# Optimization experiments

Measured on AMD Instinct MI355X. Metric: run time of the kernel, lower is better.

## Reference

```python
import jax, jax.numpy as jnp
import numpy as np

B, N, D_IN, D_OUT, R = 8, 1024, 256, 256, 4


def setup_inputs() -> dict:
    key = jax.random.key(0)
    ks = jax.random.split(key, 8)
    scale_in = 1.0 / np.sqrt(D_IN)
    scale_out = 1.0 / np.sqrt(2 * D_OUT)
    scale_g = 1.0 / np.sqrt(D_OUT)
    return {
        "node_features": jax.random.normal(ks[0], (B, N, D_IN), dtype=jnp.float32),
        "adj_matrix": jax.random.randint(ks[1], (B, R, N, N), 0, 2, dtype=jnp.int32),
        "rel_w": jax.random.uniform(ks[2], (R, D_OUT, D_IN), jnp.float32, -scale_in, scale_in),
        "rel_b": jax.random.uniform(ks[3], (R, D_OUT), jnp.float32, -scale_in, scale_in),
        "attn_w": jax.random.uniform(ks[4], (2 * D_OUT,), jnp.float32, -scale_out, scale_out),
        "attn_b": jax.random.uniform(ks[5], (), jnp.float32, -scale_out, scale_out),
        "gate_w": jax.random.uniform(ks[6], (D_OUT,), jnp.float32, -scale_g, scale_g),
        "gate_b": jax.random.uniform(ks[7], (), jnp.float32, -scale_g, scale_g),
    }


def reference(node_features, adj_matrix, rel_w, rel_b, attn_w, attn_b, gate_w, gate_b):
    # Per-relation projections: [B, R, N, D]
    feats = jnp.einsum('bni,rdi->brnd', node_features, rel_w) + rel_b[None, :, None, :]
    # attn_proj(cat([h_i, h_j])) == h_i @ w_i + h_j @ w_j + b  (linear over concat)
    d = feats.shape[-1]
    si = jnp.einsum('brnd,d->brn', feats, attn_w[:d])   # contribution of row node i
    sj = jnp.einsum('brnd,d->brn', feats, attn_w[d:])   # contribution of col node j
    score = si[:, :, :, None] + sj[:, :, None, :] + attn_b  # [B, R, N, N]
    score = jnp.where(adj_matrix == 0, jnp.float32(-1e9), score)
    attn = jax.nn.softmax(score, axis=-1)
    # Aggregate over relations: sum_r attn_r @ feats_r -> [B, N, D]
    agg = jnp.einsum('brnm,brmd->bnd', attn, feats)
    gate = jax.nn.sigmoid(jnp.einsum('bnd,d->bn', agg, gate_w) + gate_b)
    return gate[:, :, None] * agg
```

## Files before the change

kernel.cpp:

```cpp
#include <hip/hip_runtime.h>
#include <hip/hip_bf16.h>

#define B_ 8
#define N_ 1024
#define DIN 256
#define DOUT 256
#define R_ 4

typedef __attribute__((ext_vector_type(8))) short bf16x8;
typedef __attribute__((ext_vector_type(4))) float f32x4;
typedef __attribute__((ext_vector_type(4))) int i32x4;

__device__ __forceinline__ unsigned short f2bf(float f) {
    union { float f; unsigned int u; } v; v.f = f;
    unsigned int u = v.u;
    u += 0x7fffu + ((u >> 16) & 1u);
    return (unsigned short)(u >> 16);
}
__device__ __forceinline__ float bf2f(unsigned short h) {
    union { float f; unsigned int u; } v; v.u = ((unsigned int)h) << 16;
    return v.f;
}

__device__ __forceinline__ void gl_lds16(const void* g, void* l) {
    __builtin_amdgcn_global_load_lds(
        (const __attribute__((address_space(1))) unsigned int*)g,
        (__attribute__((address_space(3))) unsigned int*)l, 16, 0, 0);
}

__device__ __forceinline__ i32x4 gload4(const void* p) {
    i32x4 r;
    asm volatile("global_load_dwordx4 %0, %1, off" : "=v"(r) : "v"(p) : "memory");
    return r;
}

__global__ __launch_bounds__(256) void k0_swz(const float* __restrict__ rw,
                                              unsigned short* __restrict__ swzW) {
    int t = blockIdx.x * 256 + threadIdx.x;
    int lane = t & 63, nb = (t >> 6) & 15, ks = (t >> 10) & 7, r = t >> 13;
    int m = lane & 15, q = lane >> 4;
    const float* src = rw + ((r * DOUT + nb * 16 + m) * DIN) + ks * 32 + q * 8;
    float4 v0 = *(const float4*)src;
    float4 v1 = *(const float4*)(src + 4);
    bf16x8 o;
    o[0] = (short)f2bf(v0.x); o[1] = (short)f2bf(v0.y);
    o[2] = (short)f2bf(v0.z); o[3] = (short)f2bf(v0.w);
    o[4] = (short)f2bf(v1.x); o[5] = (short)f2bf(v1.y);
    o[6] = (short)f2bf(v1.z); o[7] = (short)f2bf(v1.w);
    *(bf16x8*)(swzW + (long)t * 8) = o;
}

__global__ __launch_bounds__(256) void k1_proj(const float* __restrict__ node,
        const unsigned short* __restrict__ swzW, const float* __restrict__ rel_b,
        const float* __restrict__ attn_w,
        unsigned short* __restrict__ fswz, unsigned short* __restrict__ ebf) {
    __shared__ unsigned short Wbuf[2][8192];
    int bid = blockIdx.x;
    int nt = bid & 15, r = (bid >> 4) & 3, b = bid >> 6;
    int w = threadIdx.x >> 6, lane = threadIdx.x & 63;
    int m = lane & 15, q = lane >> 4;
    int n0 = nt * 64 + w * 16;

    const float* Abase = node + ((b * N_ + n0 + m) * DIN) + q * 8;
    const unsigned short* Wsrc = swzW + r * 65536;

#pragma unroll
    for (int i = 0; i < 4; i++)
        gl_lds16(Wsrc + (w * 4 + i) * 512 + lane * 8, &Wbuf[0][(w * 4 + i) * 512]);

    f32x4 acc[16];
#pragma unroll
    for (int i = 0; i < 16; i++) acc[i] = (f32x4)0.0f;

    float4 a0 = *(const float4*)(Abase);
    float4 a1 = *(const float4*)(Abase + 4);

    for (int ks = 0; ks < 8; ks++) {
        int cur = ks & 1;
        __syncthreads();
        if (ks < 7) {
#pragma unroll
            for (int i = 0; i < 4; i++)
                gl_lds16(Wsrc + ((ks + 1) * 16 + w * 4 + i) * 512 + lane * 8,
                         &Wbuf[cur ^ 1][(w * 4 + i) * 512]);
        }
        bf16x8 af;
        af[0] = (short)f2bf(a0.x); af[1] = (short)f2bf(a0.y);
        af[2] = (short)f2bf(a0.z); af[3] = (short)f2bf(a0.w);
        af[4] = (short)f2bf(a1.x); af[5] = (short)f2bf(a1.y);
        af[6] = (short)f2bf(a1.z); af[7] = (short)f2bf(a1.w);
        if (ks < 7) {
            a0 = *(const float4*)(Abase + (ks + 1) * 32);
            a1 = *(const float4*)(Abase + (ks + 1) * 32 + 4);
        }
#pragma unroll
        for (int nb = 0; nb < 16; nb++) {
            bf16x8 wf = *(const bf16x8*)(&Wbuf[cur][nb * 512 + lane * 8]);
            acc[nb] = __builtin_amdgcn_mfma_f32_16x16x32_bf16(af, wf, acc[nb], 0, 0, 0);
        }
    }

    float sj0 = 0.f, sj1 = 0.f, sj2 = 0.f, sj3 = 0.f;
    float bias[16], aw[16];
#pragma unroll
    for (int nb = 0; nb < 16; nb++) {
        int d = nb * 16 + m;
        bias[nb] = rel_b[r * DOUT + d];
        aw[nb] = attn_w[DOUT + d];
        sj0 += (acc[nb][0] + bias[nb]) * aw[nb];
        sj1 += (acc[nb][1] + bias[nb]) * aw[nb];
        sj2 += (acc[nb][2] + bias[nb]) * aw[nb];
        sj3 += (acc[nb][3] + bias[nb]) * aw[nb];
    }
#pragma unroll
    for (int mk = 1; mk <= 8; mk <<= 1) {
        sj0 += __shfl_xor(sj0, mk, 64);
        sj1 += __shfl_xor(sj1, mk, 64);
        sj2 += __shfl_xor(sj2, mk, 64);
        sj3 += __shfl_xor(sj3, mk, 64);
    }
    float e0 = __expf(sj0), e1 = __expf(sj1), e2 = __expf(sj2), e3 = __expf(sj3);

    int slice = b * R_ + r;
    int js = n0 >> 5;
    int jhi = (n0 >> 4) & 1;
    int qp = jhi * 2 + (q >> 1);
    int jj0 = (q & 1) * 4;
    unsigned short* fb = fswz + ((long)(slice * 32 + js) * 16) * 512
                       + qp * 128 + m * 8 + jj0;
#pragma unroll
    for (int nb = 0; nb < 16; nb++) {
        ushort4 o;
        o.x = f2bf((acc[nb][0] + bias[nb]) * e0);
        o.y = f2bf((acc[nb][1] + bias[nb]) * e1);
        o.z = f2bf((acc[nb][2] + bias[nb]) * e2);
        o.w = f2bf((acc[nb][3] + bias[nb]) * e3);
        *(ushort4*)(fb + nb * 512) = o;
    }
    if (m == 0) {
        ushort4 o;
        o.x = f2bf(e0); o.y = f2bf(e1); o.z = f2bf(e2); o.w = f2bf(e3);
        *(ushort4*)(ebf + slice * N_ + n0 + q * 4) = o;
    }
}

#define K3_STEP(T_, SLOT_, PFSLOT_, DO_PF_, WAITN_)                            \
  {                                                                            \
    asm volatile("s_waitcnt vmcnt(" #WAITN_ ")" ::: "memory");                 \
    __builtin_amdgcn_s_barrier();                                              \
    __builtin_amdgcn_sched_barrier(0);                                         \
    if (DO_PF_) {                                                              \
      _Pragma("unroll")                                                        \
      for (int i = 0; i < 4; i++)                                              \
        gl_lds16(fsl + (size_t)((T_) + 2) * 8192 + (w * 4 + i) * 512 + lane * 8, \
                 &Gbuf[PFSLOT_][(w * 4 + i) * 512]);                           \
      adjA[PFSLOT_] = gload4(adjbase + ((T_) + 2) * 32);                       \
      adjB[PFSLOT_] = gload4(adjbase + ((T_) + 2) * 32 + 4);                   \
    }                                                                          \
    bf16x8 ev = *(const bf16x8*)(&Ebuf[(T_) * 32 + q * 8]);                    \
    i32x4 A0c = adjA[SLOT_], A1c = adjB[SLOT_];                                \
    int av[8] = {A0c.x, A0c.y, A0c.z, A0c.w, A1c.x, A1c.y, A1c.z, A1c.w};      \
    const int* ei = (const int*)&ev;                                           \
    bf16x8 af; int* afi = (int*)&af;                                           \
    _Pragma("unroll")                                                          \
    for (int p = 0; p < 4; p++) {                                              \
      unsigned int msk = (av[2 * p] ? 0xffffu : 0u)                            \
                       | (av[2 * p + 1] ? 0xffff0000u : 0u);                   \
      afi[p] = (int)(msk & 0x3F803F80u);                                       \
      int me = ei[p] & (int)msk;                                               \
      union { int i; float f; } lo, hi;                                        \
      lo.i = me << 16; hi.i = me & (int)0xffff0000u;                           \
      l += lo.f + hi.f;                                                        \
    }                                                                          \
    const unsigned short* Gb = &Gbuf[SLOT_][lane * 8];                         \
    _Pragma("unroll")                                                          \
    for (int nb = 0; nb < 16; nb++) {                                          \
      bf16x8 bfq = *(const bf16x8*)(Gb + nb * 512);                            \
      acc[nb] = __builtin_amdgcn_mfma_f32_16x16x32_bf16(af, bfq, acc[nb], 0, 0, 0); \
    }                                                                          \
  }

__global__ __launch_bounds__(256, 2) void k3_attn(const int* __restrict__ adj,
        const unsigned short* __restrict__ fswz, const unsigned short* __restrict__ ebf,
        unsigned short* __restrict__ aggN) {
    __shared__ unsigned short Gbuf[4][8192];
    __shared__ unsigned short Ebuf[1024];

    int bid = blockIdx.x;
    int slice = (bid & 7) * 4 + ((bid >> 3) & 3);
    int it = bid >> 5;
    int t = threadIdx.x, lane = t & 63, w = t >> 6;
    int m = lane & 15, q = lane >> 4;
    int i0 = it * 64 + w * 16;

    const unsigned short* fsl = fswz + (size_t)slice * (32 * 8192);
    const int* adjbase = adj + (size_t)slice * (N_ * N_)
                       + (size_t)(i0 + m) * N_ + q * 8;
    const unsigned short* esl = ebf + slice * N_;

    i32x4 adjA[4], adjB[4];

#pragma unroll
    for (int i = 0; i < 4; i++)
        gl_lds16(fsl + (w * 4 + i) * 512 + lane * 8, &Gbuf[0][(w * 4 + i) * 512]);
    if (w < 2)
        gl_lds16(esl + w * 512 + lane * 8, &Ebuf[w * 512]);
    adjA[0] = gload4(adjbase);
    adjB[0] = gload4(adjbase + 4);
#pragma unroll
    for (int i = 0; i < 4; i++)
        gl_lds16(fsl + 8192 + (w * 4 + i) * 512 + lane * 8, &Gbuf[1][(w * 4 + i) * 512]);
    adjA[1] = gload4(adjbase + 32);
    adjB[1] = gload4(adjbase + 36);

    f32x4 acc[16];
#pragma unroll
    for (int i = 0; i < 16; i++) acc[i] = (f32x4)0.0f;
    float l = 0.f;

    for (int tt = 0; tt < 28; tt += 4) {
        K3_STEP(tt + 0, 0, 2, 1, 6)
        K3_STEP(tt + 1, 1, 3, 1, 6)
        K3_STEP(tt + 2, 2, 0, 1, 6)
        K3_STEP(tt + 3, 3, 1, 1, 6)
    }
    K3_STEP(28, 0, 2, 1, 6)
    K3_STEP(29, 1, 3, 1, 6)
    K3_STEP(30, 2, 0, 0, 6)
    K3_STEP(31, 3, 1, 0, 0)

    l += __shfl_xor(l, 16, 64);
    l += __shfl_xor(l, 32, 64);
    float linv[4];
#pragma unroll
    for (int reg = 0; reg < 4; reg++) {
        float lr = __shfl(l, q * 4 + reg, 64);
        linv[reg] = (lr > 0.f) ? 1.0f / lr : 0.f;
    }
    unsigned short* ob = aggN + ((size_t)(slice * N_ + i0 + q * 4)) * DOUT + m;
#pragma unroll
    for (int nb = 0; nb < 16; nb++) {
#pragma unroll
        for (int reg = 0; reg < 4; reg++)
            ob[(size_t)reg * DOUT + nb * 16] = f2bf(acc[nb][reg] * linv[reg]);
    }
}

__global__ __launch_bounds__(256) void k4_out(const unsigned short* __restrict__ aggN,
        const float* __restrict__ gate_w, const float* __restrict__ gate_b,
        float* __restrict__ out) {
    __shared__ float red[4];
    int bid = blockIdx.x;
    int n = bid & 1023, b = bid >> 10;
    int d = threadIdx.x;
    float s = 0.f;
#pragma unroll
    for (int r = 0; r < R_; r++)
        s += bf2f(aggN[((size_t)((b * R_ + r) * N_ + n)) * DOUT + d]);
    float v = s * gate_w[d];
#pragma unroll
    for (int off = 32; off; off >>= 1) v += __shfl_down(v, off, 64);
    int lane = d & 63, wave = d >> 6;
    if (lane == 0) red[wave] = v;
    __syncthreads();
    float tot = red[0] + red[1] + red[2] + red[3];
    float g = 1.f / (1.f + __expf(-(tot + gate_b[0])));
    out[((size_t)(b * N_ + n)) * DOUT + d] = g * s;
}

extern "C" void kernel_launch(void* const* d_in, const int* in_sizes, int n_in,
                              void* d_out, int out_size, void* d_ws, size_t ws_size,
                              hipStream_t stream) {
    const float* node   = (const float*)d_in[0];
    const int*   adj    = (const int*)d_in[1];
    const float* rel_w  = (const float*)d_in[2];
    const float* rel_b  = (const float*)d_in[3];
    const float* attn_w = (const float*)d_in[4];
    const float* gate_w = (const float*)d_in[6];
    const float* gate_b = (const float*)d_in[7];
    float* out = (float*)d_out;

    char* ws = (char*)d_ws;
    unsigned short* swzW = (unsigned short*)ws;
    unsigned short* fswz = (unsigned short*)(ws + 524288);
    unsigned short* ebf  = (unsigned short*)(ws + 17301504);
    unsigned short* aggN = (unsigned short*)(ws + 17367040);

    k0_swz<<<128, 256, 0, stream>>>(rel_w, swzW);
    k1_proj<<<512, 256, 0, stream>>>(node, swzW, rel_b, attn_w, fswz, ebf);
    k3_attn<<<512, 256, 0, stream>>>(adj, fswz, ebf, aggN);
    k4_out<<<8192, 256, 0, stream>>>(aggN, gate_w, gate_b, out);
}
```

Before: 251.6 us.

## Preload adjacency tile as packed bitmask in LDS before attention loop

Before the main loop, each block now reads its 64-row adjacency tile with coalesced vector loads. It packs the tile into 32-bit bitmasks in LDS, padded to a stride of 33 words. The steady-state loop then takes its mask bits from LDS instead of issuing two strided global dwordx4 loads per step, and the vmcnt wait counts are lowered to match. The goal is better coalescing of the dominant adjacency traffic and less VGPR pressure. The trade-off is an unoverlapped preload phase plus a block barrier, and about 8 KB of extra LDS that could constrain occupancy.

```diff
diff --git a/kernel.cpp b/kernel.cpp
--- a/kernel.cpp
+++ b/kernel.cpp
@@ -26,12 +26,6 @@
     __builtin_amdgcn_global_load_lds(
         (const __attribute__((address_space(1))) unsigned int*)g,
         (__attribute__((address_space(3))) unsigned int*)l, 16, 0, 0);
-}
-
-__device__ __forceinline__ i32x4 gload4(const void* p) {
-    i32x4 r;
-    asm volatile("global_load_dwordx4 %0, %1, off" : "=v"(r) : "v"(p) : "memory");
-    return r;
 }
 
 __global__ __launch_bounds__(256) void k0_swz(const float* __restrict__ rw,
@@ -154,20 +148,18 @@
       for (int i = 0; i < 4; i++)                                              \
         gl_lds16(fsl + (size_t)((T_) + 2) * 8192 + (w * 4 + i) * 512 + lane * 8, \
                  &Gbuf[PFSLOT_][(w * 4 + i) * 512]);                           \
-      adjA[PFSLOT_] = gload4(adjbase + ((T_) + 2) * 32);                       \
-      adjB[PFSLOT_] = gload4(adjbase + ((T_) + 2) * 32 + 4);                   \
     }                                                                          \
     bf16x8 ev = *(const bf16x8*)(&Ebuf[(T_) * 32 + q * 8]);                    \
-    i32x4 A0c = adjA[SLOT_], A1c = adjB[SLOT_];                                \
-    int av[8] = {A0c.x, A0c.y, A0c.z, A0c.w, A1c.x, A1c.y, A1c.z, A1c.w};      \
+    unsigned int aw_ = AbitsW[(w * 16 + m) * 33 + (T_)];                       \
+    unsigned int ab_ = (aw_ >> (q * 8)) & 0xffu;                               \
     const int* ei = (const int*)&ev;                                           \
     bf16x8 af; int* afi = (int*)&af;                                           \
     _Pragma("unroll")                                                          \
     for (int p = 0; p < 4; p++) {                                              \
-      unsigned int msk = (av[2 * p] ? 0xffffu : 0u)                            \
-                       | (av[2 * p + 1] ? 0xffff0000u : 0u);                   \
-      afi[p] = (int)(msk & 0x3F803F80u);                                       \
-      int me = ei[p] & (int)msk;                                               \
+      unsigned int msk = (((ab_ >> (2 * p)) & 1u) ? 0xffffu : 0u)              \
+                       | (((ab_ >> (2 * p + 1)) & 1u) ? 0xffff0000u : 0u);     \
+      afi[p] = (int)(msk & 0x3F803F80u);        \
+      int me = ei[p] & (int)msk;               \
       union { int i; float f; } lo, hi;                                        \
       lo.i = me << 16; hi.i = me & (int)0xffff0000u;                           \
       l += lo.f + hi.f;                                                        \
@@ -185,6 +177,7 @@
         unsigned short* __restrict__ aggN) {
     __shared__ unsigned short Gbuf[4][8192];
     __shared__ unsigned short Ebuf[1024];
+    __shared__ unsigned int AbitsW[64 * 33];
 
     int bid = blockIdx.x;
     int slice = (bid & 7) * 4 + ((bid >> 3) & 3);
@@ -194,24 +187,40 @@
     int i0 = it * 64 + w * 16;
 
     const unsigned short* fsl = fswz + (size_t)slice * (32 * 8192);
-    const int* adjbase = adj + (size_t)slice * (N_ * N_)
-                       + (size_t)(i0 + m) * N_ + q * 8;
-    const unsigned short* esl = ebf + slice * N_;
-
-    i32x4 adjA[4], adjB[4];
+
+    ((ushort4*)Ebuf)[t] = ((const ushort4*)(ebf + slice * N_))[t];
+
+    {
+        const int* arow = adj + (size_t)slice * (N_ * N_) + (size_t)i0 * N_;
+        for (int r = 0; r < 16; r++) {
+            const int* rp = arow + (size_t)r * N_ + lane * 16;
+            i32x4 c0 = *(const i32x4*)(rp);
+            i32x4 c1 = *(const i32x4*)(rp + 4);
+            i32x4 c2 = *(const i32x4*)(rp + 8);
+            i32x4 c3 = *(const i32x4*)(rp + 12);
+            unsigned int bits =
+                  (c0.x ? 0x0001u : 0u) | (c0.y ? 0x0002u : 0u)
+                | (c0.z ? 0x0004u : 0u) | (c0.w ? 0x0008u : 0u)
+                | (c1.x ? 0x0010u : 0u) | (c1.y ? 0x0020u : 0u)
+                | (c1.z ? 0x0040u : 0u) | (c1.w ? 0x0080u : 0u)
+                | (c2.x ? 0x0100u : 0u) | (c2.y ? 0x0200u : 0u)
+                | (c2.z ? 0x0400u : 0u) | (c2.w ? 0x0800u : 0u)
+                | (c3.x ? 0x1000u : 0u) | (c3.y ? 0x2000u : 0u)
+                | (c3.z ? 0x4000u : 0u) | (c3.w ? 0x8000u : 0u);
+            unsigned int other = __shfl_xor((int)bits, 1, 64);
+            if (!(lane & 1))
+                AbitsW[(w * 16 + r) * 33 + (lane >> 1)] = bits | (other << 16);
+        }
+    }
+
+    __syncthreads();
 
 #pragma unroll
     for (int i = 0; i < 4; i++)
         gl_lds16(fsl + (w * 4 + i) * 512 + lane * 8, &Gbuf[0][(w * 4 + i) * 512]);
-    if (w < 2)
-        gl_lds16(esl + w * 512 + lane * 8, &Ebuf[w * 512]);
-    adjA[0] = gload4(adjbase);
-    adjB[0] = gload4(adjbase + 4);
 #pragma unroll
     for (int i = 0; i < 4; i++)
         gl_lds16(fsl + 8192 + (w * 4 + i) * 512 + lane * 8, &Gbuf[1][(w * 4 + i) * 512]);
-    adjA[1] = gload4(adjbase + 32);
-    adjB[1] = gload4(adjbase + 36);
 
     f32x4 acc[16];
 #pragma unroll
@@ -219,15 +228,15 @@
     float l = 0.f;
 
     for (int tt = 0; tt < 28; tt += 4) {
-        K3_STEP(tt + 0, 0, 2, 1, 6)
-        K3_STEP(tt + 1, 1, 3, 1, 6)
-        K3_STEP(tt + 2, 2, 0, 1, 6)
-        K3_STEP(tt + 3, 3, 1, 1, 6)
-    }
-    K3_STEP(28, 0, 2, 1, 6)
-    K3_STEP(29, 1, 3, 1, 6)
-    K3_STEP(30, 2, 0, 0, 6)
-    K3_STEP(31, 3, 1, 0, 0)
+        K3_STEP(tt + 0, 0, 2, 1, 4)
+        K3_STEP(tt + 1, 1, 3, 1, 4)
+        K3_STEP(tt + 2, 2, 0, 1, 4)
+        K3_STEP(tt + 3, 3, 1, 1, 4)
+    }
+    K3_STEP(28, 0, 2, 1, 4)
+    K3_STEP(29, 1, 3, 1, 4)
+    K3_STEP(30, 2, 0, 0, 4)
+    K3_STEP(31, 3, 0, 0, 0)
 
     l += __shfl_xor(l, 16, 64);
     l += __shfl_xor(l, 32, 64);
```

Measured after the change: 253.5 us. No clear change (+0.8%).

## Double rows per wave in attention kernel to reuse feature tiles

Applied to the files above, without the earlier changes.

Each wave now computes two 16-row MFMA tiles that share the same LDS feature fragments, halving the grid and the feature tile traffic per output row. Adjacency prefetch doubles per thread and the Ebuf load becomes a plain cooperative copy with a sync. This raises register pressure and cuts occupancy to one block per CU, with fewer blocks available to hide memory latency.

```diff
diff --git a/kernel.cpp b/kernel.cpp
--- a/kernel.cpp
+++ b/kernel.cpp
@@ -154,33 +154,44 @@
       for (int i = 0; i < 4; i++)                                              \
         gl_lds16(fsl + (size_t)((T_) + 2) * 8192 + (w * 4 + i) * 512 + lane * 8, \
                  &Gbuf[PFSLOT_][(w * 4 + i) * 512]);                           \
-      adjA[PFSLOT_] = gload4(adjbase + ((T_) + 2) * 32);                       \
-      adjB[PFSLOT_] = gload4(adjbase + ((T_) + 2) * 32 + 4);                   \
+      adj0A[PFSLOT_] = gload4(adjb0 + ((T_) + 2) * 32);                        \
+      adj0B[PFSLOT_] = gload4(adjb0 + ((T_) + 2) * 32 + 4);                    \
+      adj1A[PFSLOT_] = gload4(adjb1 + ((T_) + 2) * 32);                        \
+      adj1B[PFSLOT_] = gload4(adjb1 + ((T_) + 2) * 32 + 4);                    \
     }                                                                          \
     bf16x8 ev = *(const bf16x8*)(&Ebuf[(T_) * 32 + q * 8]);                    \
-    i32x4 A0c = adjA[SLOT_], A1c = adjB[SLOT_];                                \
-    int av[8] = {A0c.x, A0c.y, A0c.z, A0c.w, A1c.x, A1c.y, A1c.z, A1c.w};      \
     const int* ei = (const int*)&ev;                                           \
-    bf16x8 af; int* afi = (int*)&af;                                           \
+    i32x4 C0a = adj0A[SLOT_], C0b = adj0B[SLOT_];                              \
+    i32x4 C1a = adj1A[SLOT_], C1b = adj1B[SLOT_];                              \
+    int av0[8] = {C0a.x, C0a.y, C0a.z, C0a.w, C0b.x, C0b.y, C0b.z, C0b.w};     \
+    int av1[8] = {C1a.x, C1a.y, C1a.z, C1a.w, C1b.x, C1b.y, C1b.z, C1b.w};     \
+    bf16x8 af0, af1; int* af0i = (int*)&af0; int* af1i = (int*)&af1;           \
     _Pragma("unroll")                                                          \
     for (int p = 0; p < 4; p++) {                                              \
-      unsigned int msk = (av[2 * p] ? 0xffffu : 0u)                            \
-                       | (av[2 * p + 1] ? 0xffff0000u : 0u);                   \
-      afi[p] = (int)(msk & 0x3F803F80u);                                       \
-      int me = ei[p] & (int)msk;                                               \
-      union { int i; float f; } lo, hi;                                        \
-      lo.i = me << 16; hi.i = me & (int)0xffff0000u;                           \
-      l += lo.f + hi.f;                                                        \
+      unsigned int m0 = (av0[2 * p] ? 0xffffu : 0u)                            \
+                      | (av0[2 * p + 1] ? 0xffff0000u : 0u);                   \
+      unsigned int m1 = (av1[2 * p] ? 0xffffu : 0u)                            \
+                      | (av1[2 * p + 1] ? 0xffff0000u : 0u);                   \
+      af0i[p] = (int)(m0 & 0x3F803F80u);                   \
+      af1i[p] = (int)(m1 & 0x3F803F80u);                                       \
+      int me0 = ei[p] & (int)m0;                                               \
+      int me1 = ei[p] & (int)m1;                                               \
+      union { int i; float f; } a, b, c, d;                                    \
+      a.i = me0 << 16; b.i = me0 & (int)0xffff0000u;                           \
+      c.i = me1 << 16; d.i = me1 & (int)0xffff0000u;                           \
+      l0 += a.f + b.f;                                                         \
+      l1 += c.f + d.f;                                                         \
     }                                                                          \
     const unsigned short* Gb = &Gbuf[SLOT_][lane * 8];                         \
     _Pragma("unroll")                                                          \
     for (int nb = 0; nb < 16; nb++) {                                          \
       bf16x8 bfq = *(const bf16x8*)(Gb + nb * 512);                            \
-      acc[nb] = __builtin_amdgcn_mfma_f32_16x16x32_bf16(af, bfq, acc[nb], 0, 0, 0); \
+      acc0[nb] = __builtin_amdgcn_mfma_f32_16x16x32_bf16(af0, bfq, acc0[nb], 0, 0, 0); \
+      acc1[nb] = __builtin_amdgcn_mfma_f32_16x16x32_bf16(af1, bfq, acc1[nb], 0, 0, 0); \
     }                                                                          \
   }
 
-__global__ __launch_bounds__(256, 2) void k3_attn(const int* __restrict__ adj,
+__global__ __launch_bounds__(256, 1) void k3_attn(const int* __restrict__ adj,
         const unsigned short* __restrict__ fswz, const unsigned short* __restrict__ ebf,
         unsigned short* __restrict__ aggN) {
     __shared__ unsigned short Gbuf[4][8192];
@@ -191,58 +202,70 @@
     int it = bid >> 5;
     int t = threadIdx.x, lane = t & 63, w = t >> 6;
     int m = lane & 15, q = lane >> 4;
-    int i0 = it * 64 + w * 16;
+    int i0 = it * 128 + w * 32;
 
     const unsigned short* fsl = fswz + (size_t)slice * (32 * 8192);
-    const int* adjbase = adj + (size_t)slice * (N_ * N_)
-                       + (size_t)(i0 + m) * N_ + q * 8;
-    const unsigned short* esl = ebf + slice * N_;
-
-    i32x4 adjA[4], adjB[4];
+    const int* adjb0 = adj + (size_t)slice * (N_ * N_)
+                     + (size_t)(i0 + m) * N_ + q * 8;
+    const int* adjb1 = adjb0 + (size_t)16 * N_;
+
+    ((ushort4*)Ebuf)[t] = ((const ushort4*)(ebf + slice * N_))[t];
+    __syncthreads();
+
+    i32x4 adj0A[4], adj0B[4], adj1A[4], adj1B[4];
 
 #pragma unroll
     for (int i = 0; i < 4; i++)
         gl_lds16(fsl + (w * 4 + i) * 512 + lane * 8, &Gbuf[0][(w * 4 + i) * 512]);
-    if (w < 2)
-        gl_lds16(esl + w * 512 + lane * 8, &Ebuf[w * 512]);
-    adjA[0] = gload4(adjbase);
-    adjB[0] = gload4(adjbase + 4);
+    adj0A[0] = gload4(adjb0);
+    adj0B[0] = gload4(adjb0 + 4);
+    adj1A[0] = gload4(adjb1);
+    adj1B[0] = gload4(adjb1 + 4);
 #pragma unroll
     for (int i = 0; i < 4; i++)
         gl_lds16(fsl + 8192 + (w * 4 + i) * 512 + lane * 8, &Gbuf[1][(w * 4 + i) * 512]);
-    adjA[1] = gload4(adjbase + 32);
-    adjB[1] = gload4(adjbase + 36);
-
-    f32x4 acc[16];
-#pragma unroll
-    for (int i = 0; i < 16; i++) acc[i] = (f32x4)0.0f;
-    float l = 0.f;
+    adj0A[1] = gload4(adjb0 + 32);
+    adj0B[1] = gload4(adjb0 + 36);
+    adj1A[1] = gload4(adjb1 + 32);
+    adj1B[1] = gload4(adjb1 + 36);
+
+    f32x4 acc0[16], acc1[16];
+#pragma unroll
+    for (int i = 0; i < 16; i++) { acc0[i] = (f32x4)0.0f; acc1[i] = (f32x4)0.0f; }
+    float l0 = 0.f, l1 = 0.f;
 
     for (int tt = 0; tt < 28; tt += 4) {
-        K3_STEP(tt + 0, 0, 2, 1, 6)
-        K3_STEP(tt + 1, 1, 3, 1, 6)
-        K3_STEP(tt + 2, 2, 0, 1, 6)
-        K3_STEP(tt + 3, 3, 1, 1, 6)
-    }
-    K3_STEP(28, 0, 2, 1, 6)
-    K3_STEP(29, 1, 3, 1, 6)
-    K3_STEP(30, 2, 0, 0, 6)
-    K3_STEP(31, 3, 1, 0, 0)
-
-    l += __shfl_xor(l, 16, 64);
-    l += __shfl_xor(l, 32, 64);
-    float linv[4];
+        K3_STEP(tt + 0, 0, 2, 1, 8)
+        K3_STEP(tt + 1, 1, 3, 1, 8)
+        K3_STEP(tt + 2, 2, 0, 1, 8)
+        K3_STEP(tt + 3, 3, 1, 1, 8)
+    }
+    K3_STEP(28, 0, 2, 1, 8)
+    K3_STEP(29, 1, 3, 1, 8)
+    K3_STEP(30, 2, 0, 0, 8)
+    K3_STEP(31, 3, 0, 0, 0)
+
+    l0 += __shfl_xor(l0, 16, 64);
+    l0 += __shfl_xor(l0, 32, 64);
+    l1 += __shfl_xor(l1, 16, 64);
+    l1 += __shfl_xor(l1, 32, 64);
+    float linv0[4], linv1[4];
 #pragma unroll
     for (int reg = 0; reg < 4; reg++) {
-        float lr = __shfl(l, q * 4 + reg, 64);
-        linv[reg] = (lr > 0.f) ? 1.0f / lr : 0.f;
-    }
-    unsigned short* ob = aggN + ((size_t)(slice * N_ + i0 + q * 4)) * DOUT + m;
+        float r0 = __shfl(l0, q * 4 + reg, 64);
+        float r1 = __shfl(l1, q * 4 + reg, 64);
+        linv0[reg] = (r0 > 0.f) ? 1.0f / r0 : 0.f;
+        linv1[reg] = (r1 > 0.f) ? 1.0f / r1 : 0.f;
+    }
+    unsigned short* ob0 = aggN + ((size_t)(slice * N_ + i0 + q * 4)) * DOUT + m;
+    unsigned short* ob1 = ob0 + (size_t)16 * DOUT;
 #pragma unroll
     for (int nb = 0; nb < 16; nb++) {
 #pragma unroll
-        for (int reg = 0; reg < 4; reg++)
-            ob[(size_t)reg * DOUT + nb * 16] = f2bf(acc[nb][reg] * linv[reg]);
+        for (int reg = 0; reg < 4; reg++) {
+            ob0[(size_t)reg * DOUT + nb * 16] = f2bf(acc0[nb][reg] * linv0[reg]);
+            ob1[(size_t)reg * DOUT + nb * 16] = f2bf(acc1[nb][reg] * linv1[reg]);
+        }
     }
 }
 
@@ -288,6 +311,6 @@
 
     k0_swz<<<128, 256, 0, stream>>>(rel_w, swzW);
     k1_proj<<<512, 256, 0, stream>>>(node, swzW, rel_b, attn_w, fswz, ebf);
-    k3_attn<<<512, 256, 0, stream>>>(adj, fswz, ebf, aggN);
+    k3_attn<<<256, 256, 0, stream>>>(adj, fswz, ebf, aggN);
     k4_out<<<8192, 256, 0, stream>>>(aggN, gate_w, gate_b, out);
 }
```

New measurement: 251.6 us. No clear change (+0.0%).
